# Kernel optimization log

Hardware: AMD Instinct MI355X
Metric: run time of the kernel (lower is better)

The kernel has to match this reference:

```python
import jax, jax.numpy as jnp
import numpy as np

B, S, D, H = 4, 2048, 1024, 16
HEAD = D // H
DENOM = float(np.sqrt(D))  # NOTE: original divides by sqrt(hidden_size), not sqrt(head_size)


def setup_inputs() -> dict:
    key = jax.random.key(0)
    ks = jax.random.split(key, 5)
    scale = 1.0 / np.sqrt(D)
    return {
        "hidden_state": jax.random.normal(ks[0], (B, S, D), dtype=jnp.float32),
        "attention_mask": jnp.ones((B, S), dtype=jnp.int32),  # unused in forward (faithful to source)
        "w_q": jax.random.normal(ks[1], (D, D), dtype=jnp.float32) * scale,
        "w_k": jax.random.normal(ks[2], (D, D), dtype=jnp.float32) * scale,
        "w_v": jax.random.normal(ks[3], (D, D), dtype=jnp.float32) * scale,
        "w_o": jax.random.normal(ks[4], (D, D), dtype=jnp.float32) * scale,
    }


def _split_heads(x):
    # [B, S, D] -> [B, H, S, head]
    b, s, _ = x.shape
    return x.reshape(b, s, H, HEAD).transpose(0, 2, 1, 3)


def reference(hidden_state, attention_mask, w_q, w_k, w_v, w_o):
    # nn.Linear(bias=False): y = x @ W^T with W of shape [out, in]
    q = _split_heads(hidden_state @ w_q.T)  # [B, H, S, head]
    k = _split_heads(hidden_state @ w_k.T)
    v = _split_heads(hidden_state @ w_v.T)
    qk = jnp.einsum("bhqd,bhkd->bhqk", q, k) / DENOM  # scale = 1/sqrt(hidden_size)
    attn = jax.nn.softmax(qk, axis=-1)  # attention_mask is NOT applied (matches source)
    ctx = jnp.einsum("bhqk,bhkd->bhqd", attn, v)  # [B, H, S, head]
    ctx = ctx.transpose(0, 2, 1, 3).reshape(hidden_state.shape[0], hidden_state.shape[1], D)
    return ctx @ w_o.T
```

## Files before the change

### kernel.cpp

```cpp
#include <hip/hip_runtime.h>
#include <hip/hip_bf16.h>
#include <math.h>

typedef __bf16 bf16x8 __attribute__((ext_vector_type(8)));
typedef __bf16 bf16x2 __attribute__((ext_vector_type(2)));
typedef float f32x4 __attribute__((ext_vector_type(4)));
typedef float f32x16 __attribute__((ext_vector_type(16)));
typedef unsigned u32x2v __attribute__((ext_vector_type(2)));
typedef unsigned u32x4v __attribute__((ext_vector_type(4)));
typedef unsigned short u16;

#define QSCALE 0.04508422002778011f

__device__ __forceinline__ u16 f2b(float f) {
  union { float f; unsigned u; } x; x.f = f;
  unsigned r = x.u + 0x7fffu + ((x.u >> 16) & 1u);
  return (u16)(r >> 16);
}

__device__ __forceinline__ unsigned pkbf(float a, float b) {
  bf16x2 t = { (__bf16)a, (__bf16)b };
  return __builtin_bit_cast(unsigned, t);
}

#define GLOAD_LDS16(g, s)                                                      \
  __builtin_amdgcn_global_load_lds(                                            \
      (__attribute__((address_space(1))) void*)(void*)(g),                     \
      (__attribute__((address_space(3))) void*)(s), 16, 0, 0)

__global__ void cast_bf16_kernel(const float* __restrict__ in, u16* __restrict__ out,
                                 int n4) {
  int i = blockIdx.x * blockDim.x + threadIdx.x;
  int stride = gridDim.x * blockDim.x;
  for (; i < n4; i += stride) {
    float4 v = ((const float4*)in)[i];
    ushort4 o;
    o.x = f2b(v.x); o.y = f2b(v.y); o.z = f2b(v.z); o.w = f2b(v.w);
    ((ushort4*)out)[i] = o;
  }
}

__global__ void cast_w4_kernel(const float* __restrict__ wq, const float* __restrict__ wk,
                               const float* __restrict__ wv, const float* __restrict__ wo,
                               u16* __restrict__ wqkv, u16* __restrict__ wob) {
  const int w = blockIdx.y;
  const float* src = (w == 0) ? wq : (w == 1) ? wk : (w == 2) ? wv : wo;
  u16* dst = (w < 3) ? wqkv + (size_t)w * 1024 * 1024 : wob;
  const float scale = (w == 0) ? QSCALE : 1.0f;
  const int n4 = 1024 * 1024 / 4;
  int i = blockIdx.x * blockDim.x + threadIdx.x;
  int stride = gridDim.x * blockDim.x;
  for (; i < n4; i += stride) {
    float4 v = ((const float4*)src)[i];
    ushort4 o;
    o.x = f2b(v.x * scale); o.y = f2b(v.y * scale);
    o.z = f2b(v.z * scale); o.w = f2b(v.w * scale);
    ((ushort4*)dst)[i] = o;
  }
}

__global__ __launch_bounds__(256) void gemm_qkv(const u16* __restrict__ A,
                                                const u16* __restrict__ Bw,
                                                u16* __restrict__ Qo,
                                                u16* __restrict__ Ko,
                                                u16* __restrict__ Vt) {
  __shared__ u16 As[128 * 32];
  __shared__ u16 Bs[128 * 32];
  const int tid = threadIdx.x;
  const int wid = tid >> 6, lane = tid & 63;
  const int fr = lane & 15, fg = lane >> 4;
  const int wr = wid >> 1, wc = wid & 1;
  const int m0 = blockIdx.y * 128, n0 = blockIdx.x * 128;
  const int K = 1024;

  f32x4 acc[4][4] = {};

  for (int kt = 0; kt < K; kt += 32) {
#pragma unroll
    for (int i2 = 0; i2 < 2; ++i2) {
      int c = i2 * 256 + tid;
      int row = c >> 2, kc = c & 3;
      GLOAD_LDS16(A + (size_t)(m0 + row) * K + kt + kc * 8, (char*)As + c * 16);
      GLOAD_LDS16(Bw + (size_t)(n0 + row) * K + kt + kc * 8, (char*)Bs + c * 16);
    }
    __syncthreads();

    bf16x8 af[4], bfr[4];
#pragma unroll
    for (int m = 0; m < 4; ++m)
      af[m] = *(const bf16x8*)((const char*)As + (wr * 64 + m * 16 + fr) * 64 + fg * 16);
#pragma unroll
    for (int n = 0; n < 4; ++n)
      bfr[n] = *(const bf16x8*)((const char*)Bs + (wc * 64 + n * 16 + fr) * 64 + fg * 16);
#pragma unroll
    for (int m = 0; m < 4; ++m)
#pragma unroll
      for (int n = 0; n < 4; ++n)
        acc[m][n] = __builtin_amdgcn_mfma_f32_16x16x32_bf16(af[m], bfr[n], acc[m][n], 0, 0, 0);
    __syncthreads();
  }

  const int region = n0 >> 10;
#pragma unroll
  for (int m = 0; m < 4; ++m)
#pragma unroll
    for (int n = 0; n < 4; ++n) {
      int gr = m0 + wr * 64 + m * 16 + fg * 4;
      int gc = n0 + wc * 64 + n * 16 + fr;
      if (region == 2) {
        int vc = gc - 2048;
        int hh = vc >> 6, d = vc & 63, bb = gr >> 11, s0 = gr & 2047;
        ushort4 o;
        o.x = f2b(acc[m][n][0]); o.y = f2b(acc[m][n][1]);
        o.z = f2b(acc[m][n][2]); o.w = f2b(acc[m][n][3]);
        *(ushort4*)(Vt + (((size_t)bb * 16 + hh) * 64 + d) * 2048 + s0) = o;
      } else {
        u16* dst = (region == 0) ? Qo : Ko;
        int cc = gc & 1023;
#pragma unroll
        for (int j = 0; j < 4; ++j)
          dst[(size_t)(gr + j) * 1024 + cc] = f2b(acc[m][n][j]);
      }
    }
}

__global__ __launch_bounds__(256) void gemm_o(const u16* __restrict__ A,
                                              const u16* __restrict__ B,
                                              float* __restrict__ Cout) {
  __shared__ u16 As[128 * 32];
  __shared__ u16 Bs[128 * 32];
  const int tid = threadIdx.x;
  const int wid = tid >> 6, lane = tid & 63;
  const int fr = lane & 15, fg = lane >> 4;
  const int wr = wid >> 1, wc = wid & 1;
  const int m0 = blockIdx.y * 128, n0 = blockIdx.x * 128;
  const int K = 1024, N = 1024;

  f32x4 acc[4][4] = {};

  for (int kt = 0; kt < K; kt += 32) {
#pragma unroll
    for (int i2 = 0; i2 < 2; ++i2) {
      int c = i2 * 256 + tid;
      int row = c >> 2, kc = c & 3;
      GLOAD_LDS16(A + (size_t)(m0 + row) * K + kt + kc * 8, (char*)As + c * 16);
      GLOAD_LDS16(B + (size_t)(n0 + row) * K + kt + kc * 8, (char*)Bs + c * 16);
    }
    __syncthreads();

    bf16x8 af[4], bfr[4];
#pragma unroll
    for (int m = 0; m < 4; ++m)
      af[m] = *(const bf16x8*)((const char*)As + (wr * 64 + m * 16 + fr) * 64 + fg * 16);
#pragma unroll
    for (int n = 0; n < 4; ++n)
      bfr[n] = *(const bf16x8*)((const char*)Bs + (wc * 64 + n * 16 + fr) * 64 + fg * 16);
#pragma unroll
    for (int m = 0; m < 4; ++m)
#pragma unroll
      for (int n = 0; n < 4; ++n)
        acc[m][n] = __builtin_amdgcn_mfma_f32_16x16x32_bf16(af[m], bfr[n], acc[m][n], 0, 0, 0);
    __syncthreads();
  }

#pragma unroll
  for (int m = 0; m < 4; ++m)
#pragma unroll
    for (int n = 0; n < 4; ++n) {
      int gr = m0 + wr * 64 + m * 16 + fg * 4;
      int gc = n0 + wc * 64 + n * 16 + fr;
#pragma unroll
      for (int j = 0; j < 4; ++j)
        Cout[(size_t)(gr + j) * N + gc] = acc[m][n][j];
    }
}

__global__ __launch_bounds__(256, 2) void attn_fwd(const u16* __restrict__ Q,
                                                   const u16* __restrict__ Kg,
                                                   const u16* __restrict__ Vtg,
                                                   u16* __restrict__ O) {
  __shared__ u16 Ks[2][64 * 64];
  __shared__ u16 Vs[2][64 * 64];
  const int tid = threadIdx.x;
  const int wid = tid >> 6, lane = tid & 63;
  const int lq = lane & 31, hi = lane >> 5;
  const int id = blockIdx.x;
  const int swz = (id & 7) * 64 + (id >> 3);
  const int qb = swz & 7, bh = swz >> 3;
  const int b = bh >> 4, h = bh & 15;
  const size_t tokBase = (size_t)b * 2048 * 1024 + h * 64;
  const size_t vBase = (size_t)bh * 64 * 2048;
  const int q0 = qb * 256 + wid * 64;

  bf16x8 qfA[4], qfB[4];
#pragma unroll
  for (int s = 0; s < 4; ++s) {
    qfA[s] = *(const bf16x8*)(Q + tokBase + (size_t)(q0 + lq) * 1024 + s * 16 + hi * 8);
    qfB[s] = *(const bf16x8*)(Q + tokBase + (size_t)(q0 + 32 + lq) * 1024 + s * 16 + hi * 8);
  }

  f32x16 accA0 = {}, accA1 = {}, accB0 = {}, accB1 = {};
  f32x16 lsvA = {}, lsvB = {};

  const int skey = tid >> 3, sdc = tid & 7;
  const int sdg = sdc ^ (skey & 7);
  const int skey2 = (tid + 256) >> 3;
  const int sdg2 = sdc ^ (skey2 & 7);

#define STAGE(bb_, k0_) do {                                                          \
    GLOAD_LDS16(Kg + tokBase + (size_t)((k0_) + skey) * 1024 + sdg * 8,               \
                (char*)Ks[bb_] + tid * 16);                                           \
    GLOAD_LDS16(Kg + tokBase + (size_t)((k0_) + skey2) * 1024 + sdg2 * 8,             \
                (char*)Ks[bb_] + (tid + 256) * 16);                                   \
    GLOAD_LDS16(Vtg + vBase + (size_t)skey * 2048 + (k0_) + sdg * 8,                  \
                (char*)Vs[bb_] + tid * 16);                                           \
    GLOAD_LDS16(Vtg + vBase + (size_t)skey2 * 2048 + (k0_) + sdg2 * 8,                \
                (char*)Vs[bb_] + (tid + 256) * 16);                                   \
  } while (0)

  STAGE(0, 0);
  for (int t = 0; t < 32; ++t) {
    const int bb = t & 1;
    __syncthreads();
    if (t < 31) STAGE(bb ^ 1, (t + 1) * 64);

    f32x16 svA0 = {}, svA1 = {}, svB0 = {}, svB1 = {};
    __builtin_amdgcn_s_setprio(1);
#pragma unroll
    for (int s = 0; s < 4; ++s) {
      bf16x8 kf0 = *(const bf16x8*)((const char*)Ks[bb] + lq * 128 +
                                    ((s * 32 + hi * 16) ^ ((lq & 7) << 4)));
      bf16x8 kf1 = *(const bf16x8*)((const char*)Ks[bb] + (32 + lq) * 128 +
                                    ((s * 32 + hi * 16) ^ ((lq & 7) << 4)));
      svA0 = __builtin_amdgcn_mfma_f32_32x32x16_bf16(kf0, qfA[s], svA0, 0, 0, 0);
      svB0 = __builtin_amdgcn_mfma_f32_32x32x16_bf16(kf0, qfB[s], svB0, 0, 0, 0);
      svA1 = __builtin_amdgcn_mfma_f32_32x32x16_bf16(kf1, qfA[s], svA1, 0, 0, 0);
      svB1 = __builtin_amdgcn_mfma_f32_32x32x16_bf16(kf1, qfB[s], svB1, 0, 0, 0);
    }
    __builtin_amdgcn_s_setprio(0);

#pragma unroll
    for (int i = 0; i < 16; ++i) svA0[i] = __builtin_amdgcn_exp2f(svA0[i]);
#pragma unroll
    for (int i = 0; i < 16; ++i) svA1[i] = __builtin_amdgcn_exp2f(svA1[i]);
#pragma unroll
    for (int i = 0; i < 16; ++i) svB0[i] = __builtin_amdgcn_exp2f(svB0[i]);
#pragma unroll
    for (int i = 0; i < 16; ++i) svB1[i] = __builtin_amdgcn_exp2f(svB1[i]);
    lsvA += svA0; lsvA += svA1;
    lsvB += svB0; lsvB += svB1;

    bf16x8 paA[4], paB[4];
#pragma unroll
    for (int kb = 0; kb < 2; ++kb) {
#pragma unroll
      for (int hh = 0; hh < 2; ++hh) {
        const int rb = hh * 8;
        {
          const f32x16& pv = kb ? svA1 : svA0;
          unsigned w01 = pkbf(pv[rb + 0], pv[rb + 1]);
          unsigned w23 = pkbf(pv[rb + 2], pv[rb + 3]);
          unsigned w45 = pkbf(pv[rb + 4], pv[rb + 5]);
          unsigned w67 = pkbf(pv[rb + 6], pv[rb + 7]);
          u32x2v ra = __builtin_amdgcn_permlane32_swap(w01, w45, false, false);
          u32x2v rc = __builtin_amdgcn_permlane32_swap(w23, w67, false, false);
          u32x4v fw = { ra[0], rc[0], ra[1], rc[1] };
          paA[kb * 2 + hh] = __builtin_bit_cast(bf16x8, fw);
        }
        {
          const f32x16& pv = kb ? svB1 : svB0;
          unsigned w01 = pkbf(pv[rb + 0], pv[rb + 1]);
          unsigned w23 = pkbf(pv[rb + 2], pv[rb + 3]);
          unsigned w45 = pkbf(pv[rb + 4], pv[rb + 5]);
          unsigned w67 = pkbf(pv[rb + 6], pv[rb + 7]);
          u32x2v ra = __builtin_amdgcn_permlane32_swap(w01, w45, false, false);
          u32x2v rc = __builtin_amdgcn_permlane32_swap(w23, w67, false, false);
          u32x4v fw = { ra[0], rc[0], ra[1], rc[1] };
          paB[kb * 2 + hh] = __builtin_bit_cast(bf16x8, fw);
        }
      }
    }

    __builtin_amdgcn_s_setprio(1);
#pragma unroll
    for (int s = 0; s < 4; ++s) {
      bf16x8 bv0 = *(const bf16x8*)((const char*)Vs[bb] + lq * 128 +
                                    ((s * 32 + hi * 16) ^ ((lq & 7) << 4)));
      bf16x8 bv1 = *(const bf16x8*)((const char*)Vs[bb] + (32 + lq) * 128 +
                                    ((s * 32 + hi * 16) ^ ((lq & 7) << 4)));
      accA0 = __builtin_amdgcn_mfma_f32_32x32x16_bf16(paA[s], bv0, accA0, 0, 0, 0);
      accA1 = __builtin_amdgcn_mfma_f32_32x32x16_bf16(paA[s], bv1, accA1, 0, 0, 0);
      accB0 = __builtin_amdgcn_mfma_f32_32x32x16_bf16(paB[s], bv0, accB0, 0, 0, 0);
      accB1 = __builtin_amdgcn_mfma_f32_32x32x16_bf16(paB[s], bv1, accB1, 0, 0, 0);
    }
    __builtin_amdgcn_s_setprio(0);
  }
#undef STAGE

  float totA = 0.f, totB = 0.f;
#pragma unroll
  for (int i = 0; i < 16; ++i) { totA += lsvA[i]; totB += lsvB[i]; }
  totA += __shfl_xor(totA, 32);
  totB += __shfl_xor(totB, 32);
  const float invA = 1.0f / totA, invB = 1.0f / totB;
#pragma unroll
  for (int r = 0; r < 16; ++r) {
    const int q = (r & 3) + 8 * (r >> 2) + 4 * hi;
    const float ivA = __shfl(invA, q);
    const float ivB = __shfl(invB, q);
    const size_t rowA = (size_t)(b * 2048 + q0 + q) * 1024 + h * 64;
    const size_t rowB = (size_t)(b * 2048 + q0 + 32 + q) * 1024 + h * 64;
    O[rowA + lq]      = f2b(accA0[r] * ivA);
    O[rowA + 32 + lq] = f2b(accA1[r] * ivA);
    O[rowB + lq]      = f2b(accB0[r] * ivB);
    O[rowB + 32 + lq] = f2b(accB1[r] * ivB);
  }
}

extern "C" void kernel_launch(void* const* d_in, const int* in_sizes, int n_in,
                              void* d_out, int out_size, void* d_ws, size_t ws_size,
                              hipStream_t stream) {
  const float* hs = (const float*)d_in[0];
  const float* wq = (const float*)d_in[2];
  const float* wk = (const float*)d_in[3];
  const float* wv = (const float*)d_in[4];
  const float* wo = (const float*)d_in[5];

  const size_t TOK = 8192, DD = 1024;
  u16* hsb  = (u16*)d_ws;
  u16* wqkv = hsb + TOK * DD;
  u16* wob  = wqkv + 3 * DD * DD;
  u16* Qb   = wob + DD * DD;
  u16* Kb   = Qb + TOK * DD;
  u16* Vtg  = Kb + TOK * DD;
  u16* Cb   = Vtg + TOK * DD;

  cast_bf16_kernel<<<2048, 256, 0, stream>>>(hs, hsb, (int)(TOK * DD / 4));
  cast_w4_kernel<<<dim3(128, 4), 256, 0, stream>>>(wq, wk, wv, wo, wqkv, wob);

  gemm_qkv<<<dim3(24, 64), 256, 0, stream>>>(hsb, wqkv, Qb, Kb, Vtg);

  attn_fwd<<<dim3(512), 256, 0, stream>>>(Qb, Kb, Vtg, Cb);

  gemm_o<<<dim3(8, 64), 256, 0, stream>>>(Cb, wob, (float*)d_out);
}
```

Before: 199.6 us.

## Rewrite projection GEMMs with double-buffered LDS, swizzle, larger tiles and XCD remap

Replaces the two separate projection GEMMs with one templated kernel that uses 256x128 tiles, 512 threads and K-steps of 64. Global-to-LDS loads are double-buffered so the next tile is fetched while MFMAs run on the current one. The LDS layout is XOR-swizzled to reduce bank conflicts, and block ids are remapped so neighbouring tiles land on the same XCD for better cache reuse. The cost is 96KB of LDS per block, which limits occupancy, and hand-written waitcnt and barrier sequencing that must match the number of outstanding loads.

```diff
diff --git a/kernel.cpp b/kernel.cpp
--- a/kernel.cpp
+++ b/kernel.cpp
@@ -22,6 +22,8 @@
   bf16x2 t = { (__bf16)a, (__bf16)b };
   return __builtin_bit_cast(unsigned, t);
 }
+
+__device__ __forceinline__ int SWZ(int x) { return x ^ (((x >> 9) & 1) << 5); }
 
 #define GLOAD_LDS16(g, s)                                                      \
   __builtin_amdgcn_global_load_lds(                                            \
@@ -59,119 +61,123 @@
   }
 }
 
-__global__ __launch_bounds__(256) void gemm_qkv(const u16* __restrict__ A,
-                                                const u16* __restrict__ Bw,
-                                                u16* __restrict__ Qo,
-                                                u16* __restrict__ Ko,
-                                                u16* __restrict__ Vt) {
-  __shared__ u16 As[128 * 32];
-  __shared__ u16 Bs[128 * 32];
+template <int MODE>
+__global__ __launch_bounds__(512, 2) void gemm_big(const u16* __restrict__ A,
+                                                   const u16* __restrict__ Bw,
+                                                   u16* __restrict__ Qo,
+                                                   u16* __restrict__ Ko,
+                                                   u16* __restrict__ Vt,
+                                                   float* __restrict__ Fo,
+                                                   int nbx) {
+  __shared__ char smem[98304];
   const int tid = threadIdx.x;
   const int wid = tid >> 6, lane = tid & 63;
   const int fr = lane & 15, fg = lane >> 4;
-  const int wr = wid >> 1, wc = wid & 1;
-  const int m0 = blockIdx.y * 128, n0 = blockIdx.x * 128;
+  const int wm = wid >> 1, wn = wid & 1;
+  const int nwg = nbx * 32;
+  const int cpx = nwg >> 3;
+  const int id = blockIdx.x;
+  const int swzid = (id & 7) * cpx + (id >> 3);
+  const int bx = swzid % nbx, by = swzid / nbx;
+  const int m0 = by * 256, n0 = bx * 128;
   const int K = 1024;
 
+  const u16* asrc[4];
+  const u16* bsrc[2];
+#pragma unroll
+  for (int s = 0; s < 4; ++s) {
+    int l = SWZ((tid + s * 512) * 16);
+    asrc[s] = A + (size_t)(m0 + (l >> 7)) * K + ((l & 127) >> 1);
+  }
+#pragma unroll
+  for (int s = 0; s < 2; ++s) {
+    int l = SWZ((tid + s * 512) * 16);
+    bsrc[s] = Bw + (size_t)(n0 + (l >> 7)) * K + ((l & 127) >> 1);
+  }
+
   f32x4 acc[4][4] = {};
 
-  for (int kt = 0; kt < K; kt += 32) {
-#pragma unroll
-    for (int i2 = 0; i2 < 2; ++i2) {
-      int c = i2 * 256 + tid;
-      int row = c >> 2, kc = c & 3;
-      GLOAD_LDS16(A + (size_t)(m0 + row) * K + kt + kc * 8, (char*)As + c * 16);
-      GLOAD_LDS16(Bw + (size_t)(n0 + row) * K + kt + kc * 8, (char*)Bs + c * 16);
-    }
-    __syncthreads();
-
-    bf16x8 af[4], bfr[4];
-#pragma unroll
-    for (int m = 0; m < 4; ++m)
-      af[m] = *(const bf16x8*)((const char*)As + (wr * 64 + m * 16 + fr) * 64 + fg * 16);
-#pragma unroll
-    for (int n = 0; n < 4; ++n)
-      bfr[n] = *(const bf16x8*)((const char*)Bs + (wc * 64 + n * 16 + fr) * 64 + fg * 16);
-#pragma unroll
-    for (int m = 0; m < 4; ++m)
-#pragma unroll
-      for (int n = 0; n < 4; ++n)
-        acc[m][n] = __builtin_amdgcn_mfma_f32_16x16x32_bf16(af[m], bfr[n], acc[m][n], 0, 0, 0);
-    __syncthreads();
-  }
-
-  const int region = n0 >> 10;
+  auto issue = [&](int kt_) {
+    char* ab = smem + (kt_ & 1) * 32768;
+    char* bb = smem + 65536 + (kt_ & 1) * 16384;
+#pragma unroll
+    for (int s = 0; s < 4; ++s)
+      GLOAD_LDS16(asrc[s] + kt_ * 64, ab + (tid + s * 512) * 16);
+#pragma unroll
+    for (int s = 0; s < 2; ++s)
+      GLOAD_LDS16(bsrc[s] + kt_ * 64, bb + (tid + s * 512) * 16);
+  };
+
+  issue(0);
+  for (int kt = 0; kt < 16; ++kt) {
+    const char* ab = smem + (kt & 1) * 32768;
+    const char* bb = smem + 65536 + (kt & 1) * 16384;
+    if (kt < 15) {
+      issue(kt + 1);
+      asm volatile("s_waitcnt vmcnt(6)" ::: "memory");
+    } else {
+      asm volatile("s_waitcnt vmcnt(0)" ::: "memory");
+    }
+    asm volatile("s_barrier" ::: "memory");
+
+    bf16x8 aR[2][2], bR[2][2];
+#define LOADA(mh)                                                              \
+  _Pragma("unroll") for (int i = 0; i < 2; ++i)                                \
+  _Pragma("unroll") for (int ks = 0; ks < 2; ++ks)                             \
+    aR[i][ks] = *(const bf16x8*)(ab +                                          \
+        SWZ((wm * 64 + (mh)*32 + i * 16 + fr) * 128 + ks * 64 + fg * 16));
+#define LOADB(nh)                                                              \
+  _Pragma("unroll") for (int i = 0; i < 2; ++i)                                \
+  _Pragma("unroll") for (int ks = 0; ks < 2; ++ks)                             \
+    bR[i][ks] = *(const bf16x8*)(bb +                                          \
+        SWZ((wn * 64 + (nh)*32 + i * 16 + fr) * 128 + ks * 64 + fg * 16));
+#define MFMA8(mh, nh)                                                          \
+  __builtin_amdgcn_s_setprio(1);                                               \
+  _Pragma("unroll") for (int i = 0; i < 2; ++i)                                \
+  _Pragma("unroll") for (int j = 0; j < 2; ++j)                                \
+  _Pragma("unroll") for (int ks = 0; ks < 2; ++ks)                             \
+    acc[(mh)*2 + i][(nh)*2 + j] = __builtin_amdgcn_mfma_f32_16x16x32_bf16(     \
+        aR[i][ks], bR[j][ks], acc[(mh)*2 + i][(nh)*2 + j], 0, 0, 0);           \
+  __builtin_amdgcn_s_setprio(0);
+
+    LOADA(0) LOADB(0) MFMA8(0, 0)
+    LOADB(1) MFMA8(0, 1)
+    LOADA(1) MFMA8(1, 1)
+    LOADB(0) MFMA8(1, 0)
+#undef LOADA
+#undef LOADB
+#undef MFMA8
+
+    asm volatile("s_barrier" ::: "memory");
+  }
+
 #pragma unroll
   for (int m = 0; m < 4; ++m)
 #pragma unroll
     for (int n = 0; n < 4; ++n) {
-      int gr = m0 + wr * 64 + m * 16 + fg * 4;
-      int gc = n0 + wc * 64 + n * 16 + fr;
-      if (region == 2) {
-        int vc = gc - 2048;
-        int hh = vc >> 6, d = vc & 63, bb = gr >> 11, s0 = gr & 2047;
-        ushort4 o;
-        o.x = f2b(acc[m][n][0]); o.y = f2b(acc[m][n][1]);
-        o.z = f2b(acc[m][n][2]); o.w = f2b(acc[m][n][3]);
-        *(ushort4*)(Vt + (((size_t)bb * 16 + hh) * 64 + d) * 2048 + s0) = o;
+      int gr = m0 + wm * 64 + m * 16 + fg * 4;
+      int gc = n0 + wn * 64 + n * 16 + fr;
+      if (MODE == 1) {
+#pragma unroll
+        for (int j = 0; j < 4; ++j)
+          Fo[(size_t)(gr + j) * 1024 + gc] = acc[m][n][j];
       } else {
-        u16* dst = (region == 0) ? Qo : Ko;
-        int cc = gc & 1023;
-#pragma unroll
-        for (int j = 0; j < 4; ++j)
-          dst[(size_t)(gr + j) * 1024 + cc] = f2b(acc[m][n][j]);
+        const int region = n0 >> 10;
+        if (region == 2) {
+          int vc = gc - 2048;
+          int hh = vc >> 6, d = vc & 63, bb2 = gr >> 11, s0 = gr & 2047;
+          ushort4 o;
+          o.x = f2b(acc[m][n][0]); o.y = f2b(acc[m][n][1]);
+          o.z = f2b(acc[m][n][2]); o.w = f2b(acc[m][n][3]);
+          *(ushort4*)(Vt + (((size_t)bb2 * 16 + hh) * 64 + d) * 2048 + s0) = o;
+        } else {
+          u16* dst = (region == 0) ? Qo : Ko;
+          int cc = gc & 1023;
+#pragma unroll
+          for (int j = 0; j < 4; ++j)
+            dst[(size_t)(gr + j) * 1024 + cc] = f2b(acc[m][n][j]);
+        }
       }
-    }
-}
-
-__global__ __launch_bounds__(256) void gemm_o(const u16* __restrict__ A,
-                                              const u16* __restrict__ B,
-                                              float* __restrict__ Cout) {
-  __shared__ u16 As[128 * 32];
-  __shared__ u16 Bs[128 * 32];
-  const int tid = threadIdx.x;
-  const int wid = tid >> 6, lane = tid & 63;
-  const int fr = lane & 15, fg = lane >> 4;
-  const int wr = wid >> 1, wc = wid & 1;
-  const int m0 = blockIdx.y * 128, n0 = blockIdx.x * 128;
-  const int K = 1024, N = 1024;
-
-  f32x4 acc[4][4] = {};
-
-  for (int kt = 0; kt < K; kt += 32) {
-#pragma unroll
-    for (int i2 = 0; i2 < 2; ++i2) {
-      int c = i2 * 256 + tid;
-      int row = c >> 2, kc = c & 3;
-      GLOAD_LDS16(A + (size_t)(m0 + row) * K + kt + kc * 8, (char*)As + c * 16);
-      GLOAD_LDS16(B + (size_t)(n0 + row) * K + kt + kc * 8, (char*)Bs + c * 16);
-    }
-    __syncthreads();
-
-    bf16x8 af[4], bfr[4];
-#pragma unroll
-    for (int m = 0; m < 4; ++m)
-      af[m] = *(const bf16x8*)((const char*)As + (wr * 64 + m * 16 + fr) * 64 + fg * 16);
-#pragma unroll
-    for (int n = 0; n < 4; ++n)
-      bfr[n] = *(const bf16x8*)((const char*)Bs + (wc * 64 + n * 16 + fr) * 64 + fg * 16);
-#pragma unroll
-    for (int m = 0; m < 4; ++m)
-#pragma unroll
-      for (int n = 0; n < 4; ++n)
-        acc[m][n] = __builtin_amdgcn_mfma_f32_16x16x32_bf16(af[m], bfr[n], acc[m][n], 0, 0, 0);
-    __syncthreads();
-  }
-
-#pragma unroll
-  for (int m = 0; m < 4; ++m)
-#pragma unroll
-    for (int n = 0; n < 4; ++n) {
-      int gr = m0 + wr * 64 + m * 16 + fg * 4;
-      int gc = n0 + wc * 64 + n * 16 + fr;
-#pragma unroll
-      for (int j = 0; j < 4; ++j)
-        Cout[(size_t)(gr + j) * N + gc] = acc[m][n][j];
     }
 }
 
@@ -338,9 +344,10 @@
   cast_bf16_kernel<<<2048, 256, 0, stream>>>(hs, hsb, (int)(TOK * DD / 4));
   cast_w4_kernel<<<dim3(128, 4), 256, 0, stream>>>(wq, wk, wv, wo, wqkv, wob);
 
-  gemm_qkv<<<dim3(24, 64), 256, 0, stream>>>(hsb, wqkv, Qb, Kb, Vtg);
+  gemm_big<0><<<768, 512, 0, stream>>>(hsb, wqkv, Qb, Kb, Vtg, nullptr, 24);
 
   attn_fwd<<<dim3(512), 256, 0, stream>>>(Qb, Kb, Vtg, Cb);
 
-  gemm_o<<<dim3(8, 64), 256, 0, stream>>>(Cb, wob, (float*)d_out);
-}
+  gemm_big<1><<<256, 512, 0, stream>>>(Cb, wob, nullptr, nullptr, nullptr,
+                                       (float*)d_out, 8);
+}
```

Result: faster. 192.9 us (-3.4%).

## Rewrite QKV GEMM with 256x256 tiles, swizzled LDS and phased double buffering

Applied to the files above, without the earlier changes.

Replaces the 128x128, 4-wave QKV projection GEMM with a 512-thread kernel that computes 256x256 output tiles. The new kernel stages K=64 slices into 128KB of XOR-swizzled LDS using double buffering. The work is split into eight sub-phases that interleave global-to-LDS prefetch with MFMA work, using explicit barriers, waitcnts and setprio. A block-id swizzle groups tiles for better L2 reuse. The aim is to raise data reuse and overlap memory with compute, at the cost of much higher LDS use (one block per CU) and fragile hand-scheduled synchronisation.

```diff
diff --git a/kernel.cpp b/kernel.cpp
--- a/kernel.cpp
+++ b/kernel.cpp
@@ -27,6 +27,10 @@
   __builtin_amdgcn_global_load_lds(                                            \
       (__attribute__((address_space(1))) void*)(void*)(g),                     \
       (__attribute__((address_space(3))) void*)(s), 16, 0, 0)
+
+#define SBAR  asm volatile("s_barrier" ::: "memory")
+#define WAITL asm volatile("s_waitcnt lgkmcnt(0)" ::: "memory")
+#define SCHEDB __builtin_amdgcn_sched_barrier(0)
 
 __global__ void cast_bf16_kernel(const float* __restrict__ in, u16* __restrict__ out,
                                  int n4) {
@@ -59,69 +63,136 @@
   }
 }
 
-__global__ __launch_bounds__(256) void gemm_qkv(const u16* __restrict__ A,
-                                                const u16* __restrict__ Bw,
-                                                u16* __restrict__ Qo,
-                                                u16* __restrict__ Ko,
-                                                u16* __restrict__ Vt) {
-  __shared__ u16 As[128 * 32];
-  __shared__ u16 Bs[128 * 32];
+__global__ __launch_bounds__(512, 2) void gemm_qkv8(const u16* __restrict__ A,
+                                                    const u16* __restrict__ Bw,
+                                                    u16* __restrict__ Qo,
+                                                    u16* __restrict__ Ko,
+                                                    u16* __restrict__ Vt) {
+  __shared__ char smem[131072];
   const int tid = threadIdx.x;
   const int wid = tid >> 6, lane = tid & 63;
   const int fr = lane & 15, fg = lane >> 4;
-  const int wr = wid >> 1, wc = wid & 1;
-  const int m0 = blockIdx.y * 128, n0 = blockIdx.x * 128;
-  const int K = 1024;
-
-  f32x4 acc[4][4] = {};
-
-  for (int kt = 0; kt < K; kt += 32) {
-#pragma unroll
-    for (int i2 = 0; i2 < 2; ++i2) {
-      int c = i2 * 256 + tid;
-      int row = c >> 2, kc = c & 3;
-      GLOAD_LDS16(A + (size_t)(m0 + row) * K + kt + kc * 8, (char*)As + c * 16);
-      GLOAD_LDS16(Bw + (size_t)(n0 + row) * K + kt + kc * 8, (char*)Bs + c * 16);
-    }
-    __syncthreads();
-
-    bf16x8 af[4], bfr[4];
-#pragma unroll
-    for (int m = 0; m < 4; ++m)
-      af[m] = *(const bf16x8*)((const char*)As + (wr * 64 + m * 16 + fr) * 64 + fg * 16);
-#pragma unroll
-    for (int n = 0; n < 4; ++n)
-      bfr[n] = *(const bf16x8*)((const char*)Bs + (wc * 64 + n * 16 + fr) * 64 + fg * 16);
-#pragma unroll
-    for (int m = 0; m < 4; ++m)
-#pragma unroll
-      for (int n = 0; n < 4; ++n)
-        acc[m][n] = __builtin_amdgcn_mfma_f32_16x16x32_bf16(af[m], bfr[n], acc[m][n], 0, 0, 0);
-    __syncthreads();
-  }
+  const int wm = wid >> 2, wn = wid & 3;
+  const int id = blockIdx.x;
+  const int swzid = (id & 7) * 48 + (id >> 3);
+  const int bx = swzid % 12, by = swzid / 12;
+  const int m0 = by * 256, n0 = bx * 256;
+
+  const int sl0 = ((fg) ^ (fr & 7)) * 16;
+  const int sl1 = ((4 + fg) ^ (fr & 7)) * 16;
+
+  const int p0 = tid, p1 = tid + 512;
+  const u16* aptr0 = A + (size_t)(m0 + (p0 >> 3)) * 1024 + ((p0 & 7) ^ ((p0 >> 3) & 7)) * 8;
+  const u16* aptr1 = A + (size_t)(m0 + (p1 >> 3)) * 1024 + ((p1 & 7) ^ ((p1 >> 3) & 7)) * 8;
+  const u16* bptr0 = Bw + (size_t)(n0 + (p0 >> 3)) * 1024 + ((p0 & 7) ^ ((p0 >> 3) & 7)) * 8;
+  const u16* bptr1 = Bw + (size_t)(n0 + (p1 >> 3)) * 1024 + ((p1 & 7) ^ ((p1 >> 3) & 7)) * 8;
+
+#define STG_A(kt_, h_) do {                                                          \
+    GLOAD_LDS16(aptr0 + (h_) * 131072 + (kt_) * 64,                                  \
+                smem + (((kt_) & 1) * 2 + (h_)) * 16384 + tid * 16);                 \
+    GLOAD_LDS16(aptr1 + (h_) * 131072 + (kt_) * 64,                                  \
+                smem + (((kt_) & 1) * 2 + (h_)) * 16384 + (tid + 512) * 16);         \
+  } while (0)
+#define STG_B(kt_, h_) do {                                                          \
+    GLOAD_LDS16(bptr0 + (h_) * 131072 + (kt_) * 64,                                  \
+                smem + 65536 + (((kt_) & 1) * 2 + (h_)) * 16384 + tid * 16);         \
+    GLOAD_LDS16(bptr1 + (h_) * 131072 + (kt_) * 64,                                  \
+                smem + 65536 + (((kt_) & 1) * 2 + (h_)) * 16384 + (tid + 512) * 16); \
+  } while (0)
+
+  f32x4 acc[2][2][4][2] = {};
+  bf16x8 aR[4][2], bR[2][2];
+
+#define LDFRAG(d_, mh_, nh_) do {                                                    \
+    const char* Ab_ = smem + ((d_) * 2 + (mh_)) * 16384;                             \
+    const char* Bb_ = smem + 65536 + ((d_) * 2 + (nh_)) * 16384;                     \
+    _Pragma("unroll") for (int fm = 0; fm < 4; ++fm) {                               \
+      aR[fm][0] = *(const bf16x8*)(Ab_ + (wm * 64 + fm * 16 + fr) * 128 + sl0);      \
+      aR[fm][1] = *(const bf16x8*)(Ab_ + (wm * 64 + fm * 16 + fr) * 128 + sl1);      \
+    }                                                                                \
+    _Pragma("unroll") for (int fn = 0; fn < 2; ++fn) {                               \
+      bR[fn][0] = *(const bf16x8*)(Bb_ + (wn * 32 + fn * 16 + fr) * 128 + sl0);      \
+      bR[fn][1] = *(const bf16x8*)(Bb_ + (wn * 32 + fn * 16 + fr) * 128 + sl1);      \
+    }                                                                                \
+  } while (0)
+
+#define DOMFMA(mh_, nh_)                                                             \
+    __builtin_amdgcn_s_setprio(1);                                                   \
+    _Pragma("unroll") for (int fm = 0; fm < 4; ++fm)                                 \
+    _Pragma("unroll") for (int fn = 0; fn < 2; ++fn)                                 \
+    _Pragma("unroll") for (int ks = 0; ks < 2; ++ks)                                 \
+      acc[mh_][nh_][fm][fn] = __builtin_amdgcn_mfma_f32_16x16x32_bf16(               \
+          aR[fm][ks], bR[fn][ks], acc[mh_][nh_][fm][fn], 0, 0, 0);                   \
+    __builtin_amdgcn_s_setprio(0);
+
+#define PHASE(d_, mh_, nh_, STAGES_, WAIT_) do {                                     \
+    LDFRAG(d_, mh_, nh_);                                                            \
+    STAGES_;                                                                         \
+    WAIT_;                                                                           \
+    SBAR; WAITL; SCHEDB;                                                             \
+    DOMFMA(mh_, nh_);                                                                \
+    SBAR;                                                                            \
+  } while (0)
+
+  STG_A(0, 0); STG_A(0, 1); STG_B(0, 0); STG_B(0, 1);
+  STG_A(1, 0); STG_B(1, 0);
+  asm volatile("s_waitcnt vmcnt(4)" ::: "memory");
+  SBAR;
+
+  for (int i = 0; i < 7; ++i) {
+    const int ktA = 2 * i, ktB = 2 * i + 1;
+    PHASE(0, 0, 0, { STG_A(ktB, 1); STG_B(ktB, 1); }, {});
+    PHASE(0, 0, 1, {}, {});
+    PHASE(0, 1, 0, { STG_A(ktA + 2, 0); }, {});
+    PHASE(0, 1, 1, { STG_B(ktA + 2, 0); },
+          { asm volatile("s_waitcnt vmcnt(4)" ::: "memory"); });
+    PHASE(1, 0, 0, { STG_A(ktA + 2, 1); STG_B(ktA + 2, 1); }, {});
+    PHASE(1, 0, 1, {}, {});
+    PHASE(1, 1, 0, { STG_A(ktB + 2, 0); }, {});
+    PHASE(1, 1, 1, { STG_B(ktB + 2, 0); },
+          { asm volatile("s_waitcnt vmcnt(4)" ::: "memory"); });
+  }
+  PHASE(0, 0, 0, { STG_A(15, 1); STG_B(15, 1); }, {});
+  PHASE(0, 0, 1, {}, {});
+  PHASE(0, 1, 0, {}, {});
+  PHASE(0, 1, 1, {}, { asm volatile("s_waitcnt vmcnt(0)" ::: "memory"); });
+  PHASE(1, 0, 0, {}, {});
+  PHASE(1, 0, 1, {}, {});
+  PHASE(1, 1, 0, {}, {});
+  PHASE(1, 1, 1, {}, {});
+
+#undef PHASE
+#undef DOMFMA
+#undef LDFRAG
+#undef STG_A
+#undef STG_B
 
   const int region = n0 >> 10;
 #pragma unroll
-  for (int m = 0; m < 4; ++m)
-#pragma unroll
-    for (int n = 0; n < 4; ++n) {
-      int gr = m0 + wr * 64 + m * 16 + fg * 4;
-      int gc = n0 + wc * 64 + n * 16 + fr;
-      if (region == 2) {
-        int vc = gc - 2048;
-        int hh = vc >> 6, d = vc & 63, bb = gr >> 11, s0 = gr & 2047;
-        ushort4 o;
-        o.x = f2b(acc[m][n][0]); o.y = f2b(acc[m][n][1]);
-        o.z = f2b(acc[m][n][2]); o.w = f2b(acc[m][n][3]);
-        *(ushort4*)(Vt + (((size_t)bb * 16 + hh) * 64 + d) * 2048 + s0) = o;
-      } else {
-        u16* dst = (region == 0) ? Qo : Ko;
-        int cc = gc & 1023;
-#pragma unroll
-        for (int j = 0; j < 4; ++j)
-          dst[(size_t)(gr + j) * 1024 + cc] = f2b(acc[m][n][j]);
-      }
-    }
+  for (int mh = 0; mh < 2; ++mh)
+#pragma unroll
+    for (int nh = 0; nh < 2; ++nh)
+#pragma unroll
+      for (int fm = 0; fm < 4; ++fm)
+#pragma unroll
+        for (int fn = 0; fn < 2; ++fn) {
+          int gr = m0 + mh * 128 + wm * 64 + fm * 16 + fg * 4;
+          int gc = n0 + nh * 128 + wn * 32 + fn * 16 + fr;
+          f32x4 v = acc[mh][nh][fm][fn];
+          if (region == 2) {
+            int vc = gc - 2048;
+            int hh = vc >> 6, d = vc & 63, bb2 = gr >> 11, s0 = gr & 2047;
+            ushort4 o;
+            o.x = f2b(v[0]); o.y = f2b(v[1]); o.z = f2b(v[2]); o.w = f2b(v[3]);
+            *(ushort4*)(Vt + (((size_t)bb2 * 16 + hh) * 64 + d) * 2048 + s0) = o;
+          } else {
+            u16* dst = (region == 0) ? Qo : Ko;
+            int cc = gc & 1023;
+#pragma unroll
+            for (int j = 0; j < 4; ++j)
+              dst[(size_t)(gr + j) * 1024 + cc] = f2b(v[j]);
+          }
+        }
 }
 
 __global__ __launch_bounds__(256) void gemm_o(const u16* __restrict__ A,
@@ -338,7 +409,7 @@
   cast_bf16_kernel<<<2048, 256, 0, stream>>>(hs, hsb, (int)(TOK * DD / 4));
   cast_w4_kernel<<<dim3(128, 4), 256, 0, stream>>>(wq, wk, wv, wo, wqkv, wob);
 
-  gemm_qkv<<<dim3(24, 64), 256, 0, stream>>>(hsb, wqkv, Qb, Kb, Vtg);
+  gemm_qkv8<<<384, 512, 0, stream>>>(hsb, wqkv, Qb, Kb, Vtg);
 
   attn_fwd<<<dim3(512), 256, 0, stream>>>(Qb, Kb, Vtg, Cb);
 
```

Measured after the change: 198.2 us. No clear change (-0.7%).

## Double-buffer GEMM LDS tiles with async prefetch and merge GEMM kernels

Applied to the files above, without the earlier changes.

Both projection GEMMs now share one templated kernel that double-buffers the A and B LDS tiles. The next k-tile is issued via global_load_lds before computing on the current one, with explicit vmcnt waits and barriers in place of the full syncthreads pair. MFMA issue priority is raised with s_setprio during the compute section. This aims to hide global load latency behind MFMA work, at the cost of doubled LDS per block, which may reduce occupancy.

```diff
diff --git a/kernel.cpp b/kernel.cpp
--- a/kernel.cpp
+++ b/kernel.cpp
@@ -27,6 +27,10 @@
   __builtin_amdgcn_global_load_lds(                                            \
       (__attribute__((address_space(1))) void*)(void*)(g),                     \
       (__attribute__((address_space(3))) void*)(s), 16, 0, 0)
+
+#define VMCNT4 asm volatile("s_waitcnt vmcnt(4)" ::: "memory")
+#define VMCNT0 asm volatile("s_waitcnt vmcnt(0)" ::: "memory")
+#define SBAR   __builtin_amdgcn_s_barrier()
 
 __global__ void cast_bf16_kernel(const float* __restrict__ in, u16* __restrict__ out,
                                  int n4) {
@@ -59,13 +63,14 @@
   }
 }
 
-__global__ __launch_bounds__(256) void gemm_qkv(const u16* __restrict__ A,
-                                                const u16* __restrict__ Bw,
-                                                u16* __restrict__ Qo,
-                                                u16* __restrict__ Ko,
-                                                u16* __restrict__ Vt) {
-  __shared__ u16 As[128 * 32];
-  __shared__ u16 Bs[128 * 32];
+template <int OUT_MODE>
+__global__ __launch_bounds__(256) void gemm_nt(const u16* __restrict__ A,
+                                               const u16* __restrict__ B,
+                                               void* __restrict__ O0,
+                                               u16* __restrict__ Ko,
+                                               u16* __restrict__ Vt) {
+  __shared__ u16 As[2][128 * 32];
+  __shared__ u16 Bs[2][128 * 32];
   const int tid = threadIdx.x;
   const int wid = tid >> 6, lane = tid & 63;
   const int fr = lane & 15, fg = lane >> 4;
@@ -73,105 +78,75 @@
   const int m0 = blockIdx.y * 128, n0 = blockIdx.x * 128;
   const int K = 1024;
 
+  const int srow = tid >> 2, skc = tid & 3;
+  const int srow2 = (tid + 256) >> 2;
+
+#define STAGE_G(t_) do {                                                             \
+    const int d_ = (t_) & 1;                                                         \
+    GLOAD_LDS16(A + (size_t)(m0 + srow) * K + (t_) * 32 + skc * 8,                   \
+                (char*)As[d_] + tid * 16);                                           \
+    GLOAD_LDS16(A + (size_t)(m0 + srow2) * K + (t_) * 32 + skc * 8,                  \
+                (char*)As[d_] + (tid + 256) * 16);                                   \
+    GLOAD_LDS16(B + (size_t)(n0 + srow) * K + (t_) * 32 + skc * 8,                   \
+                (char*)Bs[d_] + tid * 16);                                           \
+    GLOAD_LDS16(B + (size_t)(n0 + srow2) * K + (t_) * 32 + skc * 8,                  \
+                (char*)Bs[d_] + (tid + 256) * 16);                                   \
+  } while (0)
+
   f32x4 acc[4][4] = {};
 
-  for (int kt = 0; kt < K; kt += 32) {
-#pragma unroll
-    for (int i2 = 0; i2 < 2; ++i2) {
-      int c = i2 * 256 + tid;
-      int row = c >> 2, kc = c & 3;
-      GLOAD_LDS16(A + (size_t)(m0 + row) * K + kt + kc * 8, (char*)As + c * 16);
-      GLOAD_LDS16(Bw + (size_t)(n0 + row) * K + kt + kc * 8, (char*)Bs + c * 16);
-    }
-    __syncthreads();
+  STAGE_G(0);
+  for (int t = 0; t < 32; ++t) {
+    const int d = t & 1;
+    if (t < 31) { STAGE_G(t + 1); VMCNT4; }
+    else        { VMCNT0; }
+    SBAR;
 
     bf16x8 af[4], bfr[4];
 #pragma unroll
     for (int m = 0; m < 4; ++m)
-      af[m] = *(const bf16x8*)((const char*)As + (wr * 64 + m * 16 + fr) * 64 + fg * 16);
+      af[m] = *(const bf16x8*)((const char*)As[d] + (wr * 64 + m * 16 + fr) * 64 + fg * 16);
 #pragma unroll
     for (int n = 0; n < 4; ++n)
-      bfr[n] = *(const bf16x8*)((const char*)Bs + (wc * 64 + n * 16 + fr) * 64 + fg * 16);
+      bfr[n] = *(const bf16x8*)((const char*)Bs[d] + (wc * 64 + n * 16 + fr) * 64 + fg * 16);
+    __builtin_amdgcn_s_setprio(1);
 #pragma unroll
     for (int m = 0; m < 4; ++m)
 #pragma unroll
       for (int n = 0; n < 4; ++n)
         acc[m][n] = __builtin_amdgcn_mfma_f32_16x16x32_bf16(af[m], bfr[n], acc[m][n], 0, 0, 0);
-    __syncthreads();
-  }
-
-  const int region = n0 >> 10;
+    __builtin_amdgcn_s_setprio(0);
+    SBAR;
+  }
+#undef STAGE_G
+
 #pragma unroll
   for (int m = 0; m < 4; ++m)
 #pragma unroll
     for (int n = 0; n < 4; ++n) {
       int gr = m0 + wr * 64 + m * 16 + fg * 4;
       int gc = n0 + wc * 64 + n * 16 + fr;
-      if (region == 2) {
-        int vc = gc - 2048;
-        int hh = vc >> 6, d = vc & 63, bb = gr >> 11, s0 = gr & 2047;
-        ushort4 o;
-        o.x = f2b(acc[m][n][0]); o.y = f2b(acc[m][n][1]);
-        o.z = f2b(acc[m][n][2]); o.w = f2b(acc[m][n][3]);
-        *(ushort4*)(Vt + (((size_t)bb * 16 + hh) * 64 + d) * 2048 + s0) = o;
+      if (OUT_MODE == 0) {
+#pragma unroll
+        for (int j = 0; j < 4; ++j)
+          ((float*)O0)[(size_t)(gr + j) * 1024 + gc] = acc[m][n][j];
       } else {
-        u16* dst = (region == 0) ? Qo : Ko;
-        int cc = gc & 1023;
-#pragma unroll
-        for (int j = 0; j < 4; ++j)
-          dst[(size_t)(gr + j) * 1024 + cc] = f2b(acc[m][n][j]);
+        const int region = n0 >> 10;
+        if (region == 2) {
+          int vc = gc - 2048;
+          int hh = vc >> 6, dd = vc & 63, bb2 = gr >> 11, s0 = gr & 2047;
+          ushort4 o;
+          o.x = f2b(acc[m][n][0]); o.y = f2b(acc[m][n][1]);
+          o.z = f2b(acc[m][n][2]); o.w = f2b(acc[m][n][3]);
+          *(ushort4*)(Vt + (((size_t)bb2 * 16 + hh) * 64 + dd) * 2048 + s0) = o;
+        } else {
+          u16* dst = (region == 0) ? (u16*)O0 : Ko;
+          int cc = gc & 1023;
+#pragma unroll
+          for (int j = 0; j < 4; ++j)
+            dst[(size_t)(gr + j) * 1024 + cc] = f2b(acc[m][n][j]);
+        }
       }
-    }
-}
-
-__global__ __launch_bounds__(256) void gemm_o(const u16* __restrict__ A,
-                                              const u16* __restrict__ B,
-                                              float* __restrict__ Cout) {
-  __shared__ u16 As[128 * 32];
-  __shared__ u16 Bs[128 * 32];
-  const int tid = threadIdx.x;
-  const int wid = tid >> 6, lane = tid & 63;
-  const int fr = lane & 15, fg = lane >> 4;
-  const int wr = wid >> 1, wc = wid & 1;
-  const int m0 = blockIdx.y * 128, n0 = blockIdx.x * 128;
-  const int K = 1024, N = 1024;
-
-  f32x4 acc[4][4] = {};
-
-  for (int kt = 0; kt < K; kt += 32) {
-#pragma unroll
-    for (int i2 = 0; i2 < 2; ++i2) {
-      int c = i2 * 256 + tid;
-      int row = c >> 2, kc = c & 3;
-      GLOAD_LDS16(A + (size_t)(m0 + row) * K + kt + kc * 8, (char*)As + c * 16);
-      GLOAD_LDS16(B + (size_t)(n0 + row) * K + kt + kc * 8, (char*)Bs + c * 16);
-    }
-    __syncthreads();
-
-    bf16x8 af[4], bfr[4];
-#pragma unroll
-    for (int m = 0; m < 4; ++m)
-      af[m] = *(const bf16x8*)((const char*)As + (wr * 64 + m * 16 + fr) * 64 + fg * 16);
-#pragma unroll
-    for (int n = 0; n < 4; ++n)
-      bfr[n] = *(const bf16x8*)((const char*)Bs + (wc * 64 + n * 16 + fr) * 64 + fg * 16);
-#pragma unroll
-    for (int m = 0; m < 4; ++m)
-#pragma unroll
-      for (int n = 0; n < 4; ++n)
-        acc[m][n] = __builtin_amdgcn_mfma_f32_16x16x32_bf16(af[m], bfr[n], acc[m][n], 0, 0, 0);
-    __syncthreads();
-  }
-
-#pragma unroll
-  for (int m = 0; m < 4; ++m)
-#pragma unroll
-    for (int n = 0; n < 4; ++n) {
-      int gr = m0 + wr * 64 + m * 16 + fg * 4;
-      int gc = n0 + wc * 64 + n * 16 + fr;
-#pragma unroll
-      for (int j = 0; j < 4; ++j)
-        Cout[(size_t)(gr + j) * N + gc] = acc[m][n][j];
     }
 }
 
@@ -338,9 +313,9 @@
   cast_bf16_kernel<<<2048, 256, 0, stream>>>(hs, hsb, (int)(TOK * DD / 4));
   cast_w4_kernel<<<dim3(128, 4), 256, 0, stream>>>(wq, wk, wv, wo, wqkv, wob);
 
-  gemm_qkv<<<dim3(24, 64), 256, 0, stream>>>(hsb, wqkv, Qb, Kb, Vtg);
+  gemm_nt<1><<<dim3(24, 64), 256, 0, stream>>>(hsb, wqkv, Qb, Kb, Vtg);
 
   attn_fwd<<<dim3(512), 256, 0, stream>>>(Qb, Kb, Vtg, Cb);
 
-  gemm_o<<<dim3(8, 64), 256, 0, stream>>>(Cb, wob, (float*)d_out);
-}
+  gemm_nt<0><<<dim3(8, 64), 256, 0, stream>>>(Cb, wob, d_out, nullptr, nullptr);
+}
```

After: 206.5 us. 3.4% more time.
